# Optimization experiments

Hardware: AMD Instinct MI355X
Metric: run time of the kernel (lower is better)

The kernel has to match this reference:

```python
import jax, jax.numpy as jnp
import numpy as np

B, Z, H, T = 256, 512, 1024, 512   # batch, z_size, hidden (conductor==decoder), num_tokens
L, N = 16, 16                      # num_levels, notes_per_bar


def setup_inputs() -> dict:
    key = jax.random.key(0)
    ks = jax.random.split(key, 16)
    s = 0.05  # weight init scale
    rn = lambda k, shp, sc=1.0: sc * jax.random.normal(k, shp, dtype=jnp.float32)
    return {
        "z": rn(ks[0], (B, L * N, 1, Z)),
        "dec_h0": rn(ks[1], (L, B, H)),
        "dec_c0": rn(ks[2], (L, B, H)),
        # linear_in (computed but unused by the original forward)
        "lin_in_W": rn(ks[3], (Z, Z), s), "lin_in_b": rn(ks[4], (Z,), s),
        # conductor LSTM (input Z -> hidden H), PyTorch gate order i,f,g,o
        "cond_Wih": rn(ks[5], (4 * H, Z), s), "cond_Whh": rn(ks[6], (4 * H, H), s),
        "cond_bih": rn(ks[7], (4 * H,), s), "cond_bhh": rn(ks[8], (4 * H,), s),
        # decoder LSTM (input T+H -> hidden H)
        "dec_Wih": rn(ks[9], (4 * H, T + H), s), "dec_Whh": rn(ks[10], (4 * H, H), s),
        "dec_bih": rn(ks[11], (4 * H,), s), "dec_bhh": rn(ks[12], (4 * H,), s),
        # output projection
        "out_W": rn(ks[13], (T, H), s), "out_b": rn(ks[14], (T,), s),
    }


def _lstm_cell(x, h, c, Wih, Whh, b):
    gates = x @ Wih.T + h @ Whh.T + b            # [B, 4H]
    i, f, g, o = jnp.split(gates, 4, axis=-1)
    c = jax.nn.sigmoid(f) * c + jax.nn.sigmoid(i) * jnp.tanh(g)
    h = jax.nn.sigmoid(o) * jnp.tanh(c)
    return h, c


def reference(z, dec_h0, dec_c0, lin_in_W, lin_in_b,
              cond_Wih, cond_Whh, cond_bih, cond_bhh,
              dec_Wih, dec_Whh, dec_bih, dec_bhh, out_W, out_b):
    Bsz = z.shape[0]
    Tt = out_b.shape[0]
    Hh = cond_Whh.shape[1]

    _unused = z @ lin_in_W.T + lin_in_b  # linear_in output is discarded in the source

    cond_b = cond_bih + cond_bhh
    dec_b = dec_bih + dec_bhh

    # conductor consumes z[:, L*level, 0, :] for each level
    z_lv = jnp.transpose(z[:, jnp.arange(L) * L, 0, :], (1, 0, 2))  # [L, B, Z]

    def level_step(carry, xs):
        ch, cc = carry
        zl, dh, dc = xs
        ch, cc = _lstm_cell(zl, ch, cc, cond_Wih, cond_Whh, cond_b)
        emb = ch  # [B, H], fixed conductor embedding for this bar

        def note_step(c2, _):
            note, dh2, dc2 = c2
            inp = jnp.concatenate([emb, note], axis=-1)  # [B, H+T]
            dh2, dc2 = _lstm_cell(inp, dh2, dc2, dec_Wih, dec_Whh, dec_b)
            out = jax.nn.sigmoid(dh2 @ out_W.T + out_b)  # [B, T]
            return (out, dh2, dc2), out

        note0 = jnp.zeros((Bsz, Tt), dtype=z.dtype)
        _, outs = jax.lax.scan(note_step, (note0, dh, dc), None, length=N)  # [N, B, T]
        return (ch, cc), outs

    h0 = jnp.zeros((Bsz, Hh), dtype=z.dtype)
    _, all_outs = jax.lax.scan(level_step, (h0, h0), (z_lv, dec_h0, dec_c0))  # [L, N, B, T]
    notes = jnp.transpose(all_outs, (2, 0, 1, 3)).reshape(Bsz, L * N, Tt)
    return notes
```

## Files before the change

kernel.cpp:

```cpp
#include <hip/hip_runtime.h>

typedef __bf16 bf16;
typedef __attribute__((ext_vector_type(8))) __bf16 bf16x8;
typedef __attribute__((ext_vector_type(4))) float f32x4;
typedef __attribute__((ext_vector_type(4))) unsigned short u16x4;

__device__ __forceinline__ void gload_lds16(const void* g, void* l) {
  __builtin_amdgcn_global_load_lds(
      (const __attribute__((address_space(1))) void*)g,
      (__attribute__((address_space(3))) void*)l, 16, 0, 0);
}

__device__ __forceinline__ float sigmoidf_(float x) { return 1.0f / (1.0f + expf(-x)); }

__device__ __forceinline__ float bf2f(unsigned short u) {
  union { unsigned int i; float f; } v;
  v.i = ((unsigned int)u) << 16;
  return v.f;
}
__device__ __forceinline__ unsigned short f2bfbits(float x) {
  union { bf16 b; unsigned short u; } v;
  v.b = (bf16)x;
  return v.u;
}

#define SB() __builtin_amdgcn_sched_barrier(0)
#define MFMA16(a, b, c) __builtin_amdgcn_mfma_f32_16x16x32_bf16(a, b, c, 0, 0, 0)

template<int MODE>
__global__ __launch_bounds__(512, 2)
void gemm8(const bf16* __restrict__ A, int lda,
           const bf16* __restrict__ Bw, int K,
           bf16* __restrict__ Cb,
           const bf16* __restrict__ X, const float* __restrict__ bias,
           float* __restrict__ cst, bf16* __restrict__ hout, int ldh) {
  extern __shared__ __align__(16) char smem_raw[];
  bf16* lsA = (bf16*)smem_raw;
  bf16* lsB = lsA + 32768;

  const int tid = threadIdx.x;
  const int lane = tid & 63;
  const int wave = tid >> 6;
  const int wm = wave >> 2, wn = wave & 3;

  const int bid = blockIdx.x;
  const int wgid = (bid & 7) * 32 + (bid >> 3);
  const int m0 = (wgid >> 4) * 256, n0 = (wgid & 15) * 256;

  const int nkt = K >> 6;

  const int srow = tid >> 2;
  const int scol = (tid & 3) * 8;
  const bf16* gAs = A + (size_t)(m0 + srow) * lda + scol;
  const bf16* gBs = Bw + (size_t)(n0 + srow) * K + scol;

  auto stA = [&](int kt, int ks) {
    bf16* d = lsA + (kt & 1) * 16384 + ks * 8192 + tid * 8;
    const bf16* s = gAs + (size_t)kt * 64 + ks * 32;
    gload_lds16(s, d);
    gload_lds16(s + (size_t)128 * lda, d + 4096);
  };
  auto stB = [&](int kt, int ks) {
    bf16* d = lsB + (kt & 1) * 16384 + ks * 8192 + tid * 8;
    const bf16* s = gBs + (size_t)kt * 64 + ks * 32;
    gload_lds16(s, d);
    gload_lds16(s + (size_t)128 * K, d + 4096);
  };

  const int aoff = (wm * 128 + (lane & 15)) * 32 + (lane >> 4) * 8;
  const int boff = (wn * 64 + (lane & 15)) * 32 + (lane >> 4) * 8;

  f32x4 acc[8][4] = {};

  stA(0, 0); stB(0, 0);
  stA(0, 1); stB(0, 1);
  stA(1, 0); stB(1, 0);
  asm volatile("s_waitcnt vmcnt(8)" ::: "memory");

#define PHASE(REGION_A, REGION_B, STAGE_STMT, WAIT_STMT)                      \
  do {                                                                        \
    SB();                                                                     \
    __builtin_amdgcn_s_barrier();                                             \
    SB();                                                                     \
    bf16x8 av[8], bv[4];                                                      \
    _Pragma("unroll")                                                         \
    for (int f = 0; f < 8; ++f)                                               \
      av[f] = *(const bf16x8*)&(REGION_A)[aoff + f * 512];                    \
    _Pragma("unroll")                                                         \
    for (int g = 0; g < 4; ++g)                                               \
      bv[g] = *(const bf16x8*)&(REGION_B)[boff + g * 512];                    \
    STAGE_STMT;                                                               \
    asm volatile("s_waitcnt lgkmcnt(0)" ::: "memory");                        \
    SB();                                                                     \
    __builtin_amdgcn_s_setprio(1);                                            \
    _Pragma("unroll")                                                         \
    for (int f = 0; f < 8; ++f)                                               \
      _Pragma("unroll")                                                       \
      for (int g = 0; g < 4; ++g)                                             \
        acc[f][g] = MFMA16(av[f], bv[g], acc[f][g]);                          \
    __builtin_amdgcn_s_setprio(0);                                            \
    WAIT_STMT;                                                                \
  } while (0)

  for (int t = 0; t < nkt; t += 2) {
    const bool pre = (t + 2 < nkt);
    const bf16* A00 = lsA;
    const bf16* A01 = lsA + 8192;
    const bf16* A10 = lsA + 16384;
    const bf16* A11 = lsA + 24576;
    const bf16* B00 = lsB;
    const bf16* B01 = lsB + 8192;
    const bf16* B10 = lsB + 16384;
    const bf16* B11 = lsB + 24576;

    PHASE(A00, B00,
          { stA(t + 1, 1); stB(t + 1, 1); },
          { if (pre) asm volatile("s_waitcnt vmcnt(8)" ::: "memory");
            else     asm volatile("s_waitcnt vmcnt(0)" ::: "memory"); });
    PHASE(A01, B01,
          { if (pre) { stA(t + 2, 0); stB(t + 2, 0); } },
          { if (pre) asm volatile("s_waitcnt vmcnt(8)" ::: "memory"); });
    PHASE(A10, B10,
          { if (pre) { stA(t + 2, 1); stB(t + 2, 1); } },
          { if (pre) asm volatile("s_waitcnt vmcnt(8)" ::: "memory"); });
    PHASE(A11, B11,
          { if (pre) { stA(t + 3, 0); stB(t + 3, 0); } },
          { if (pre) asm volatile("s_waitcnt vmcnt(8)" ::: "memory"); });
  }
#undef PHASE

  const int jj = lane & 15;
  const int rb = m0 + wm * 128 + ((lane >> 4) << 2);
  const int q = (n0 >> 6) + wn;
  if constexpr (MODE == 0) {
#pragma unroll
    for (int f = 0; f < 8; ++f)
#pragma unroll
      for (int r = 0; r < 4; ++r) {
        u16x4 pk;
        pk[0] = f2bfbits(acc[f][0][r]);
        pk[1] = f2bfbits(acc[f][1][r]);
        pk[2] = f2bfbits(acc[f][2][r]);
        pk[3] = f2bfbits(acc[f][3][r]);
        *(u16x4*)&Cb[(size_t)(rb + f * 16 + r) * 4096 + q * 64 + jj * 4] = pk;
      }
  } else {
    const int j = q * 16 + jj;
    const f32x4 bq = *(const f32x4*)&bias[q * 64 + jj * 4];
#pragma unroll
    for (int f = 0; f < 8; ++f) {
#pragma unroll
      for (int r = 0; r < 4; ++r) {
        const int row = rb + f * 16 + r;
        const u16x4 xv = *(const u16x4*)&X[(size_t)row * 4096 + q * 64 + jj * 4];
        const float gi = acc[f][0][r] + bf2f(xv[0]) + bq[0];
        const float gf = acc[f][1][r] + bf2f(xv[1]) + bq[1];
        const float gg = acc[f][2][r] + bf2f(xv[2]) + bq[2];
        const float go = acc[f][3][r] + bf2f(xv[3]) + bq[3];
        const size_t ci = (size_t)row * 1024 + j;
        const float cn = sigmoidf_(gf) * cst[ci] + sigmoidf_(gi) * tanhf(gg);
        cst[ci] = cn;
        hout[(size_t)row * ldh + j] = (bf16)(sigmoidf_(go) * tanhf(cn));
      }
    }
  }
}

template<int BM, int BN, int WM, int WN, int MODE>
__global__ __launch_bounds__(WM * WN * 64)
void gemm_bt(const bf16* __restrict__ A, int lda,
             const bf16* __restrict__ Bw, int ldb,
             float* __restrict__ C, int ldc, int K,
             const float* __restrict__ outb, float* __restrict__ dout,
             bf16* __restrict__ anote, int nstep) {
  constexpr int BK = 64;
  constexpr int THREADS = WM * WN * 64;
  constexpr int SM = BM / WM, SN = BN / WN;
  constexpr int FM = SM / 16, FN = SN / 16;

  __shared__ __align__(16) bf16 lsA[BM * BK];
  __shared__ __align__(16) bf16 lsB[BN * BK];

  const int tid = threadIdx.x;
  const int lane = tid & 63;
  const int wave = tid >> 6;
  const int wm = wave / WN, wn = wave % WN;
  const int m0 = blockIdx.y * BM;
  const int n0 = blockIdx.x * BN;

  f32x4 acc[FM][FN] = {};

  const bf16* gA = A + (size_t)m0 * lda;
  const bf16* gB = Bw + (size_t)n0 * ldb;

  for (int k0 = 0; k0 < K; k0 += BK) {
#pragma unroll
    for (int i = 0; i < (BM * 8) / THREADS; ++i) {
      int idx = i * THREADS + tid;
      gload_lds16(gA + (size_t)(idx >> 3) * lda + k0 + (idx & 7) * 8, &lsA[idx * 8]);
    }
#pragma unroll
    for (int i = 0; i < (BN * 8) / THREADS; ++i) {
      int idx = i * THREADS + tid;
      gload_lds16(gB + (size_t)(idx >> 3) * ldb + k0 + (idx & 7) * 8, &lsB[idx * 8]);
    }
    __syncthreads();

#pragma unroll
    for (int kk = 0; kk < BK; kk += 32) {
      bf16x8 av[FM], bv[FN];
#pragma unroll
      for (int i = 0; i < FM; ++i)
        av[i] = *(const bf16x8*)&lsA[(wm * SM + i * 16 + (lane & 15)) * BK + kk + (lane >> 4) * 8];
#pragma unroll
      for (int j = 0; j < FN; ++j)
        bv[j] = *(const bf16x8*)&lsB[(wn * SN + j * 16 + (lane & 15)) * BK + kk + (lane >> 4) * 8];
#pragma unroll
      for (int i = 0; i < FM; ++i)
#pragma unroll
        for (int j = 0; j < FN; ++j)
          acc[i][j] = MFMA16(av[i], bv[j], acc[i][j]);
    }
    __syncthreads();
  }

#pragma unroll
  for (int i = 0; i < FM; ++i) {
#pragma unroll
    for (int j = 0; j < FN; ++j) {
      const int col = n0 + wn * SN + j * 16 + (lane & 15);
      const int rbase = m0 + wm * SM + i * 16 + ((lane >> 4) << 2);
#pragma unroll
      for (int r = 0; r < 4; ++r) {
        const int row = rbase + r;
        float v = acc[i][j][r];
        if constexpr (MODE == 0) {
          C[(size_t)row * ldc + col] = v;
        } else {
          v = sigmoidf_(v + outb[col]);
          const int l = row >> 8, b = row & 255;
          dout[((size_t)(b * 256 + l * 16 + nstep)) * 512 + col] = v;
          anote[(size_t)row * 1536 + col] = (bf16)v;
        }
      }
    }
  }
}

template<int BM, int BJ, int WM, int WJ>
__global__ __launch_bounds__(WM * WJ * 64, 2)
void gemm_cell(const bf16* __restrict__ A, int lda,
               const bf16* __restrict__ Bw,
               const bf16* __restrict__ X,
               const float* __restrict__ bias,
               float* __restrict__ cst,
               bf16* __restrict__ hout, int ldh, int K) {
  constexpr int BK = 64;
  constexpr int THREADS = WM * WJ * 64;
  constexpr int BN = BJ * 64;
  constexpr int SM = BM / WM;
  constexpr int TJ = BJ / WJ;
  constexpr int FM = SM / 16;

  __shared__ __align__(16) bf16 lsA[BM * BK];
  __shared__ __align__(16) bf16 lsB[BN * BK];

  const int tid = threadIdx.x;
  const int lane = tid & 63;
  const int wave = tid >> 6;
  const int wm = wave / WJ, wj = wave % WJ;
  const int m0 = blockIdx.y * BM;
  const int qb = blockIdx.x * BJ;

  f32x4 acc[FM][TJ][4] = {};

  const bf16* gA = A + (size_t)m0 * lda;
  const bf16* gB = Bw + (size_t)(qb * 64) * K;

  for (int k0 = 0; k0 < K; k0 += BK) {
#pragma unroll
    for (int i = 0; i < (BM * 8) / THREADS; ++i) {
      int idx = i * THREADS + tid;
      gload_lds16(gA + (size_t)(idx >> 3) * lda + k0 + (idx & 7) * 8, &lsA[idx * 8]);
    }
#pragma unroll
    for (int i = 0; i < (BN * 8) / THREADS; ++i) {
      int idx = i * THREADS + tid;
      gload_lds16(gB + (size_t)(idx >> 3) * K + k0 + (idx & 7) * 8, &lsB[idx * 8]);
    }
    __syncthreads();

#pragma unroll
    for (int kk = 0; kk < BK; kk += 32) {
      bf16x8 av[FM], bv[TJ][4];
#pragma unroll
      for (int i = 0; i < FM; ++i)
        av[i] = *(const bf16x8*)&lsA[(wm * SM + i * 16 + (lane & 15)) * BK + kk + (lane >> 4) * 8];
#pragma unroll
      for (int t = 0; t < TJ; ++t)
#pragma unroll
        for (int g = 0; g < 4; ++g)
          bv[t][g] = *(const bf16x8*)
              &lsB[((wj * TJ + t) * 64 + g * 16 + (lane & 15)) * BK + kk + (lane >> 4) * 8];
#pragma unroll
      for (int i = 0; i < FM; ++i)
#pragma unroll
        for (int t = 0; t < TJ; ++t)
#pragma unroll
          for (int g = 0; g < 4; ++g)
            acc[i][t][g] = MFMA16(av[i], bv[t][g], acc[i][t][g]);
    }
    __syncthreads();
  }

#pragma unroll
  for (int i = 0; i < FM; ++i) {
#pragma unroll
    for (int t = 0; t < TJ; ++t) {
      const int q = qb + wj * TJ + t;
      const int jj = lane & 15;
      const int j = q * 16 + jj;
      const int rbase = m0 + wm * SM + i * 16 + ((lane >> 4) << 2);
      const f32x4 bq = *(const f32x4*)&bias[q * 64 + jj * 4];
#pragma unroll
      for (int r = 0; r < 4; ++r) {
        const int row = rbase + r;
        const u16x4 xv = *(const u16x4*)&X[(size_t)row * 4096 + q * 64 + jj * 4];
        const float gi = acc[i][t][0][r] + bf2f(xv[0]) + bq[0];
        const float gf = acc[i][t][1][r] + bf2f(xv[1]) + bq[1];
        const float gg = acc[i][t][2][r] + bf2f(xv[2]) + bq[2];
        const float go = acc[i][t][3][r] + bf2f(xv[3]) + bq[3];
        const size_t ci = (size_t)row * 1024 + j;
        const float c = sigmoidf_(gf) * cst[ci] + sigmoidf_(gi) * tanhf(gg);
        cst[ci] = c;
        hout[(size_t)row * ldh + j] = (bf16)(sigmoidf_(go) * tanhf(c));
      }
    }
  }
}


__global__ void conv_f32_bf16(const float* __restrict__ src, bf16* __restrict__ dst, int n) {
  int idx = blockIdx.x * 256 + threadIdx.x;
  if (idx < n) dst[idx] = (bf16)src[idx];
}

__device__ __forceinline__ int p_src_row(int n) {
  int q = n >> 6, gate = (n >> 4) & 3, jj = n & 15;
  return gate * 1024 + q * 16 + jj;
}

__global__ void pack_w_dec(const float* __restrict__ wih, const float* __restrict__ whh,
                           bf16* __restrict__ dst) {
  int idx = blockIdx.x * 256 + threadIdx.x;
  int n = idx / 1536, c = idx - n * 1536;
  int r = p_src_row(n);
  float v = (c < 512) ? wih[(size_t)r * 1536 + 1024 + c] : whh[(size_t)r * 1024 + (c - 512)];
  dst[idx] = (bf16)v;
}

__global__ void pack_w_emb(const float* __restrict__ wih, bf16* __restrict__ dst) {
  int idx = blockIdx.x * 256 + threadIdx.x;
  int n = idx >> 10, c = idx & 1023;
  dst[idx] = (bf16)wih[(size_t)p_src_row(n) * 1536 + c];
}

__global__ void pack_w_perm(const float* __restrict__ src, bf16* __restrict__ dst, int Kw) {
  int idx = blockIdx.x * 256 + threadIdx.x;
  int n = idx / Kw, c = idx - n * Kw;
  dst[idx] = (bf16)src[(size_t)p_src_row(n) * Kw + c];
}

__global__ void pack_bias(const float* __restrict__ bih, const float* __restrict__ bhh,
                          float* __restrict__ dst) {
  int n = blockIdx.x * 256 + threadIdx.x;
  int q = n >> 6, jj = (n >> 2) & 15, g = n & 3;
  int r = g * 1024 + q * 16 + jj;
  dst[n] = bih[r] + bhh[r];
}

__global__ void pack_zb(const float* __restrict__ z, bf16* __restrict__ dst) {
  int idx = blockIdx.x * 256 + threadIdx.x;
  int m = idx >> 9, k = idx & 511;
  int l = m >> 8, b = m & 255;
  dst[idx] = (bf16)z[((size_t)b * 256 + 16 * l) * 512 + k];
}

__global__ void init_cond(float* __restrict__ cc, bf16* __restrict__ hz0) {
  int idx = blockIdx.x * 256 + threadIdx.x;
  cc[idx] = 0.f;
  hz0[idx] = (bf16)0.f;
}

__global__ void init_state(const float* __restrict__ h0, const float* __restrict__ c0,
                           bf16* __restrict__ Abuf, float* __restrict__ cdec) {
  int idx = blockIdx.x * 256 + threadIdx.x;
  int m = idx / 1536, c = idx - m * 1536;
  if (c < 512) {
    Abuf[idx] = (bf16)0.f;
  } else {
    int j = c - 512;
    size_t s = (size_t)m * 1024 + j;
    Abuf[idx] = (bf16)h0[s];
    cdec[s] = c0[s];
  }
}

extern "C" void kernel_launch(void* const* d_in, const int* in_sizes, int n_in,
                              void* d_out, int out_size, void* d_ws, size_t ws_size,
                              hipStream_t stream) {
  const float* z        = (const float*)d_in[0];
  const float* dec_h0   = (const float*)d_in[1];
  const float* dec_c0   = (const float*)d_in[2];
  const float* cond_Wih = (const float*)d_in[5];
  const float* cond_Whh = (const float*)d_in[6];
  const float* cond_bih = (const float*)d_in[7];
  const float* cond_bhh = (const float*)d_in[8];
  const float* dec_Wih  = (const float*)d_in[9];
  const float* dec_Whh  = (const float*)d_in[10];
  const float* dec_bih  = (const float*)d_in[11];
  const float* dec_bhh  = (const float*)d_in[12];
  const float* out_W    = (const float*)d_in[13];
  const float* out_b    = (const float*)d_in[14];
  float* out = (float*)d_out;

  char* ws = (char*)d_ws;
  size_t off = 0;
  auto alloc = [&](size_t bytes) {
    void* p = ws + off;
    off += (bytes + 255) & ~(size_t)255;
    return p;
  };
  bf16* E     = (bf16*)alloc(4096ull * 4096 * 2);
  bf16* Xz    = (bf16*)alloc(4096ull * 4096 * 2);
  float* cdec = (float*)alloc(4096ull * 1024 * 4);
  bf16* Ab0   = (bf16*)alloc(4096ull * 1536 * 2);
  bf16* Ab1   = (bf16*)alloc(4096ull * 1536 * 2);
  bf16* Wd    = (bf16*)alloc(4096ull * 1536 * 2);
  bf16* We    = (bf16*)alloc(4096ull * 1024 * 2);
  bf16* Wcih  = (bf16*)alloc(4096ull * 512 * 2);
  bf16* Wchh  = (bf16*)alloc(4096ull * 1024 * 2);
  bf16* Wo    = (bf16*)alloc(512ull * 1024 * 2);
  float* cc   = (float*)alloc(256ull * 1024 * 4);
  bf16* emb   = (bf16*)alloc(4096ull * 1024 * 2);
  bf16* Zb    = (bf16*)alloc(4096ull * 512 * 2);
  bf16* hz0   = (bf16*)alloc(256ull * 1024 * 2);
  float* bdP  = (float*)alloc(4096ull * 4);
  float* bcP  = (float*)alloc(4096ull * 4);

  dim3 b256(256);

  hipFuncSetAttribute(reinterpret_cast<const void*>(&gemm8<0>),
                      hipFuncAttributeMaxDynamicSharedMemorySize, 131072);
  hipFuncSetAttribute(reinterpret_cast<const void*>(&gemm8<1>),
                      hipFuncAttributeMaxDynamicSharedMemorySize, 131072);

  pack_w_perm<<<4096 * 512 / 256, b256, 0, stream>>>(cond_Wih, Wcih, 512);
  pack_w_perm<<<4096 * 1024 / 256, b256, 0, stream>>>(cond_Whh, Wchh, 1024);
  conv_f32_bf16<<<(512 * 1024 + 255) / 256, b256, 0, stream>>>(out_W, Wo, 512 * 1024);
  pack_w_dec<<<4096 * 1536 / 256, b256, 0, stream>>>(dec_Wih, dec_Whh, Wd);
  pack_w_emb<<<4096 * 1024 / 256, b256, 0, stream>>>(dec_Wih, We);
  pack_bias<<<16, b256, 0, stream>>>(dec_bih, dec_bhh, bdP);
  pack_bias<<<16, b256, 0, stream>>>(cond_bih, cond_bhh, bcP);
  pack_zb<<<4096 * 512 / 256, b256, 0, stream>>>(z, Zb);
  init_cond<<<256 * 1024 / 256, b256, 0, stream>>>(cc, hz0);
  init_state<<<4096 * 1536 / 256, b256, 0, stream>>>(dec_h0, dec_c0, Ab0, cdec);

  gemm8<0><<<256, 512, 131072, stream>>>(Zb, 512, Wcih, 512, Xz,
                                         nullptr, nullptr, nullptr, nullptr, 0);

  for (int l = 0; l < 16; ++l) {
    const bf16* hprev = (l == 0) ? hz0 : (emb + (size_t)(l - 1) * 256 * 1024);
    gemm_cell<32, 2, 2, 2><<<dim3(32, 8), dim3(256), 0, stream>>>(
        hprev, 1024, Wchh, Xz + (size_t)l * 256 * 4096, bcP,
        cc, emb + (size_t)l * 256 * 1024, 1024, 1024);
  }

  gemm8<0><<<256, 512, 131072, stream>>>(emb, 1024, We, 1024, E,
                                         nullptr, nullptr, nullptr, nullptr, 0);

  for (int n = 0; n < 16; ++n) {
    bf16* Sc = (n & 1) ? Ab1 : Ab0;
    bf16* Sn = (n & 1) ? Ab0 : Ab1;
    gemm8<1><<<256, 512, 131072, stream>>>(Sc, 1536, Wd, 1536, nullptr,
                                           E, bdP, cdec, Sn + 512, 1536);
    gemm_bt<128, 64, 2, 2, 1><<<dim3(512 / 64, 4096 / 128), dim3(256), 0, stream>>>(
        Sn + 512, 1536, Wo, 1024, nullptr, 0, 1024, out_b, out, Sn, n);
  }
}
```

Measured before the change: 1.757 ms.

## Swizzle LDS layout, use 4-stage K32 pipeline, and vectorize pack kernels

Rewrites the gemm8 main loop so each iteration handles one K=32 slice, cycling through four LDS stages with a prefetch distance of two, in place of the paired-phase double buffer. The global-to-LDS column slot is XOR-swizzled by row, with matching reads, to cut LDS bank conflicts on the fragment loads. All weight packing and state init kernels are also vectorized to process four floats per thread. The tradeoff is a barrier on every K=32 step and more complex indexing.

Result: no change. 1.734 ms (-1.3%).

```diff
diff --git a/kernel.cpp b/kernel.cpp
--- a/kernel.cpp
+++ b/kernel.cpp
@@ -36,7 +36,7 @@
            float* __restrict__ cst, bf16* __restrict__ hout, int ldh) {
   extern __shared__ __align__(16) char smem_raw[];
   bf16* lsA = (bf16*)smem_raw;
-  bf16* lsB = lsA + 32768;
+  bf16* lsB = lsA + 4 * 8192;
 
   const int tid = threadIdx.x;
   const int lane = tid & 63;
@@ -47,87 +47,60 @@
   const int wgid = (bid & 7) * 32 + (bid >> 3);
   const int m0 = (wgid >> 4) * 256, n0 = (wgid & 15) * 256;
 
-  const int nkt = K >> 6;
+  const int nkt = K >> 5;
 
   const int srow = tid >> 2;
-  const int scol = (tid & 3) * 8;
+  const int scol = ((tid & 3) ^ ((srow >> 1) & 3)) * 8;
   const bf16* gAs = A + (size_t)(m0 + srow) * lda + scol;
   const bf16* gBs = Bw + (size_t)(n0 + srow) * K + scol;
 
-  auto stA = [&](int kt, int ks) {
-    bf16* d = lsA + (kt & 1) * 16384 + ks * 8192 + tid * 8;
-    const bf16* s = gAs + (size_t)kt * 64 + ks * 32;
+  auto stA = [&](int kt) {
+    bf16* d = lsA + (kt & 3) * 8192 + tid * 8;
+    const bf16* s = gAs + (size_t)kt * 32;
     gload_lds16(s, d);
     gload_lds16(s + (size_t)128 * lda, d + 4096);
   };
-  auto stB = [&](int kt, int ks) {
-    bf16* d = lsB + (kt & 1) * 16384 + ks * 8192 + tid * 8;
-    const bf16* s = gBs + (size_t)kt * 64 + ks * 32;
+  auto stB = [&](int kt) {
+    bf16* d = lsB + (kt & 3) * 8192 + tid * 8;
+    const bf16* s = gBs + (size_t)kt * 32;
     gload_lds16(s, d);
     gload_lds16(s + (size_t)128 * K, d + 4096);
   };
 
-  const int aoff = (wm * 128 + (lane & 15)) * 32 + (lane >> 4) * 8;
-  const int boff = (wn * 64 + (lane & 15)) * 32 + (lane >> 4) * 8;
+  const int sw = ((lane & 15) >> 1) & 3;
+  const int rslot = ((lane >> 4) ^ sw) * 8;
+  const int abase = (wm * 128 + (lane & 15)) * 32 + rslot;
+  const int bbase = (wn * 64 + (lane & 15)) * 32 + rslot;
 
   f32x4 acc[8][4] = {};
 
-  stA(0, 0); stB(0, 0);
-  stA(0, 1); stB(0, 1);
-  stA(1, 0); stB(1, 0);
-  asm volatile("s_waitcnt vmcnt(8)" ::: "memory");
-
-#define PHASE(REGION_A, REGION_B, STAGE_STMT, WAIT_STMT)                      \
-  do {                                                                        \
-    SB();                                                                     \
-    __builtin_amdgcn_s_barrier();                                             \
-    SB();                                                                     \
-    bf16x8 av[8], bv[4];                                                      \
-    _Pragma("unroll")                                                         \
-    for (int f = 0; f < 8; ++f)                                               \
-      av[f] = *(const bf16x8*)&(REGION_A)[aoff + f * 512];                    \
-    _Pragma("unroll")                                                         \
-    for (int g = 0; g < 4; ++g)                                               \
-      bv[g] = *(const bf16x8*)&(REGION_B)[boff + g * 512];                    \
-    STAGE_STMT;                                                               \
-    asm volatile("s_waitcnt lgkmcnt(0)" ::: "memory");                        \
-    SB();                                                                     \
-    __builtin_amdgcn_s_setprio(1);                                            \
-    _Pragma("unroll")                                                         \
-    for (int f = 0; f < 8; ++f)                                               \
-      _Pragma("unroll")                                                       \
-      for (int g = 0; g < 4; ++g)                                             \
-        acc[f][g] = MFMA16(av[f], bv[g], acc[f][g]);                          \
-    __builtin_amdgcn_s_setprio(0);                                            \
-    WAIT_STMT;                                                                \
-  } while (0)
-
-  for (int t = 0; t < nkt; t += 2) {
-    const bool pre = (t + 2 < nkt);
-    const bf16* A00 = lsA;
-    const bf16* A01 = lsA + 8192;
-    const bf16* A10 = lsA + 16384;
-    const bf16* A11 = lsA + 24576;
-    const bf16* B00 = lsB;
-    const bf16* B01 = lsB + 8192;
-    const bf16* B10 = lsB + 16384;
-    const bf16* B11 = lsB + 24576;
-
-    PHASE(A00, B00,
-          { stA(t + 1, 1); stB(t + 1, 1); },
-          { if (pre) asm volatile("s_waitcnt vmcnt(8)" ::: "memory");
-            else     asm volatile("s_waitcnt vmcnt(0)" ::: "memory"); });
-    PHASE(A01, B01,
-          { if (pre) { stA(t + 2, 0); stB(t + 2, 0); } },
-          { if (pre) asm volatile("s_waitcnt vmcnt(8)" ::: "memory"); });
-    PHASE(A10, B10,
-          { if (pre) { stA(t + 2, 1); stB(t + 2, 1); } },
-          { if (pre) asm volatile("s_waitcnt vmcnt(8)" ::: "memory"); });
-    PHASE(A11, B11,
-          { if (pre) { stA(t + 3, 0); stB(t + 3, 0); } },
-          { if (pre) asm volatile("s_waitcnt vmcnt(8)" ::: "memory"); });
-  }
-#undef PHASE
+  stA(0); stB(0); stA(1); stB(1);
+  asm volatile("s_waitcnt vmcnt(4)" ::: "memory");
+
+  for (int t = 0; t < nkt; ++t) {
+    SB();
+    __builtin_amdgcn_s_barrier();
+    SB();
+    const bf16* pA = lsA + (t & 3) * 8192;
+    const bf16* pB = lsB + (t & 3) * 8192;
+    bf16x8 av[8], bv[4];
+#pragma unroll
+    for (int f = 0; f < 8; ++f) av[f] = *(const bf16x8*)&pA[abase + f * 512];
+#pragma unroll
+    for (int g = 0; g < 4; ++g) bv[g] = *(const bf16x8*)&pB[bbase + g * 512];
+    if (t + 2 < nkt) { stA(t + 2); stB(t + 2); }
+    asm volatile("s_waitcnt lgkmcnt(0)" ::: "memory");
+    SB();
+    __builtin_amdgcn_s_setprio(1);
+#pragma unroll
+    for (int f = 0; f < 8; ++f)
+#pragma unroll
+      for (int g = 0; g < 4; ++g)
+        acc[f][g] = MFMA16(av[f], bv[g], acc[f][g]);
+    __builtin_amdgcn_s_setprio(0);
+    if (t + 2 < nkt)      asm volatile("s_waitcnt vmcnt(4)" ::: "memory");
+    else if (t + 1 < nkt) asm volatile("s_waitcnt vmcnt(0)" ::: "memory");
+  }
 
   const int jj = lane & 15;
   const int rb = m0 + wm * 128 + ((lane >> 4) << 2);
@@ -340,9 +313,11 @@
 }
 
 
-__global__ void conv_f32_bf16(const float* __restrict__ src, bf16* __restrict__ dst, int n) {
-  int idx = blockIdx.x * 256 + threadIdx.x;
-  if (idx < n) dst[idx] = (bf16)src[idx];
+__device__ __forceinline__ u16x4 f4_to_bf4(f32x4 v) {
+  u16x4 o;
+  o[0] = f2bfbits(v[0]); o[1] = f2bfbits(v[1]);
+  o[2] = f2bfbits(v[2]); o[3] = f2bfbits(v[3]);
+  return o;
 }
 
 __device__ __forceinline__ int p_src_row(int n) {
@@ -350,25 +325,31 @@
   return gate * 1024 + q * 16 + jj;
 }
 
+__global__ void conv_f32_bf16_4(const float* __restrict__ src, bf16* __restrict__ dst) {
+  int idx = (blockIdx.x * 256 + threadIdx.x) * 4;
+  *(u16x4*)&dst[idx] = f4_to_bf4(*(const f32x4*)&src[idx]);
+}
+
 __global__ void pack_w_dec(const float* __restrict__ wih, const float* __restrict__ whh,
                            bf16* __restrict__ dst) {
-  int idx = blockIdx.x * 256 + threadIdx.x;
+  int idx = (blockIdx.x * 256 + threadIdx.x) * 4;
   int n = idx / 1536, c = idx - n * 1536;
   int r = p_src_row(n);
-  float v = (c < 512) ? wih[(size_t)r * 1536 + 1024 + c] : whh[(size_t)r * 1024 + (c - 512)];
-  dst[idx] = (bf16)v;
+  const float* s = (c < 512) ? &wih[(size_t)r * 1536 + 1024 + c]
+                             : &whh[(size_t)r * 1024 + (c - 512)];
+  *(u16x4*)&dst[idx] = f4_to_bf4(*(const f32x4*)s);
 }
 
 __global__ void pack_w_emb(const float* __restrict__ wih, bf16* __restrict__ dst) {
-  int idx = blockIdx.x * 256 + threadIdx.x;
+  int idx = (blockIdx.x * 256 + threadIdx.x) * 4;
   int n = idx >> 10, c = idx & 1023;
-  dst[idx] = (bf16)wih[(size_t)p_src_row(n) * 1536 + c];
+  *(u16x4*)&dst[idx] = f4_to_bf4(*(const f32x4*)&wih[(size_t)p_src_row(n) * 1536 + c]);
 }
 
 __global__ void pack_w_perm(const float* __restrict__ src, bf16* __restrict__ dst, int Kw) {
-  int idx = blockIdx.x * 256 + threadIdx.x;
+  int idx = (blockIdx.x * 256 + threadIdx.x) * 4;
   int n = idx / Kw, c = idx - n * Kw;
-  dst[idx] = (bf16)src[(size_t)p_src_row(n) * Kw + c];
+  *(u16x4*)&dst[idx] = f4_to_bf4(*(const f32x4*)&src[(size_t)p_src_row(n) * Kw + c]);
 }
 
 __global__ void pack_bias(const float* __restrict__ bih, const float* __restrict__ bhh,
@@ -380,29 +361,31 @@
 }
 
 __global__ void pack_zb(const float* __restrict__ z, bf16* __restrict__ dst) {
-  int idx = blockIdx.x * 256 + threadIdx.x;
+  int idx = (blockIdx.x * 256 + threadIdx.x) * 4;
   int m = idx >> 9, k = idx & 511;
   int l = m >> 8, b = m & 255;
-  dst[idx] = (bf16)z[((size_t)b * 256 + 16 * l) * 512 + k];
+  *(u16x4*)&dst[idx] =
+      f4_to_bf4(*(const f32x4*)&z[((size_t)b * 256 + 16 * l) * 512 + k]);
 }
 
 __global__ void init_cond(float* __restrict__ cc, bf16* __restrict__ hz0) {
-  int idx = blockIdx.x * 256 + threadIdx.x;
-  cc[idx] = 0.f;
-  hz0[idx] = (bf16)0.f;
+  int idx = (blockIdx.x * 256 + threadIdx.x) * 4;
+  *(f32x4*)&cc[idx] = f32x4{0.f, 0.f, 0.f, 0.f};
+  *(u16x4*)&hz0[idx] = u16x4{0, 0, 0, 0};
 }
 
 __global__ void init_state(const float* __restrict__ h0, const float* __restrict__ c0,
                            bf16* __restrict__ Abuf, float* __restrict__ cdec) {
-  int idx = blockIdx.x * 256 + threadIdx.x;
+  int idx = (blockIdx.x * 256 + threadIdx.x) * 4;
   int m = idx / 1536, c = idx - m * 1536;
   if (c < 512) {
-    Abuf[idx] = (bf16)0.f;
+    *(u16x4*)&Abuf[idx] = u16x4{0, 0, 0, 0};
   } else {
     int j = c - 512;
     size_t s = (size_t)m * 1024 + j;
-    Abuf[idx] = (bf16)h0[s];
-    cdec[s] = c0[s];
+    f32x4 h = *(const f32x4*)&h0[s];
+    *(u16x4*)&Abuf[idx] = f4_to_bf4(h);
+    *(f32x4*)&cdec[s] = *(const f32x4*)&c0[s];
   }
 }
 
@@ -455,16 +438,16 @@
   hipFuncSetAttribute(reinterpret_cast<const void*>(&gemm8<1>),
                       hipFuncAttributeMaxDynamicSharedMemorySize, 131072);
 
-  pack_w_perm<<<4096 * 512 / 256, b256, 0, stream>>>(cond_Wih, Wcih, 512);
-  pack_w_perm<<<4096 * 1024 / 256, b256, 0, stream>>>(cond_Whh, Wchh, 1024);
-  conv_f32_bf16<<<(512 * 1024 + 255) / 256, b256, 0, stream>>>(out_W, Wo, 512 * 1024);
-  pack_w_dec<<<4096 * 1536 / 256, b256, 0, stream>>>(dec_Wih, dec_Whh, Wd);
-  pack_w_emb<<<4096 * 1024 / 256, b256, 0, stream>>>(dec_Wih, We);
+  pack_w_perm<<<4096 * 512 / 1024, b256, 0, stream>>>(cond_Wih, Wcih, 512);
+  pack_w_perm<<<4096 * 1024 / 1024, b256, 0, stream>>>(cond_Whh, Wchh, 1024);
+  conv_f32_bf16_4<<<512 * 1024 / 1024, b256, 0, stream>>>(out_W, Wo);
+  pack_w_dec<<<4096 * 1536 / 1024, b256, 0, stream>>>(dec_Wih, dec_Whh, Wd);
+  pack_w_emb<<<4096 * 1024 / 1024, b256, 0, stream>>>(dec_Wih, We);
   pack_bias<<<16, b256, 0, stream>>>(dec_bih, dec_bhh, bdP);
   pack_bias<<<16, b256, 0, stream>>>(cond_bih, cond_bhh, bcP);
-  pack_zb<<<4096 * 512 / 256, b256, 0, stream>>>(z, Zb);
-  init_cond<<<256 * 1024 / 256, b256, 0, stream>>>(cc, hz0);
-  init_state<<<4096 * 1536 / 256, b256, 0, stream>>>(dec_h0, dec_c0, Ab0, cdec);
+  pack_zb<<<4096 * 512 / 1024, b256, 0, stream>>>(z, Zb);
+  init_cond<<<256 * 1024 / 1024, b256, 0, stream>>>(cc, hz0);
+  init_state<<<4096 * 1536 / 1024, b256, 0, stream>>>(dec_h0, dec_c0, Ab0, cdec);
 
   gemm8<0><<<256, 512, 131072, stream>>>(Zb, 512, Wcih, 512, Xz,
                                          nullptr, nullptr, nullptr, nullptr, 0);
```
